# Optimization experiments

Measured on AMD Instinct MI355X. Metric: run time of the kernel, lower is better.

## Reference

```python
import jax, jax.numpy as jnp
import numpy as np

N = 100000   # nodes
E = 1600000  # edges
R = 20       # relations
B = 8        # bases
F_IN = 32
H = 32
F_OUT = 32


def _rel_layer(x, src, dst, etypes, V, a, w_loop, bias, activation=None):
    """DGL RelGraphConv with basis decomposition, sum aggregation, self-loop, bias.

    message m_e = x[src_e] @ W_{r_e}, W_r = sum_b a[r,b] V[b]; h_v = sum_{e->v} m_e
    Since messages are linear in x, aggregate x[src] per (dst, rel) segment first,
    then apply the relation weights once per node: same math, far less traffic.
    """
    W = jnp.einsum('rb,bio->rio', a, V)                       # [R, in, out]
    seg = dst.astype(jnp.int32) * R + etypes.astype(jnp.int32)  # [E]
    agg = jax.ops.segment_sum(x[src], seg, num_segments=N * R)  # [N*R, in]
    agg = agg.reshape(N, R, -1)
    h = jnp.einsum('nri,rio->no', agg, W) + x @ w_loop + bias   # [N, out]
    if activation is not None:
        h = activation(h)
    return h


def setup_inputs() -> dict:
    key = jax.random.key(0)
    ks = jax.random.split(key, 10)
    s = 1.0 / np.sqrt(F_IN)
    return {
        'x': jax.random.normal(ks[0], (N, F_IN), dtype=jnp.float32),
        'src': jax.random.randint(ks[1], (E,), 0, N, dtype=jnp.int32),
        'dst': jax.random.randint(ks[2], (E,), 0, N, dtype=jnp.int32),
        'etypes': jax.random.randint(ks[3], (E,), 0, R, dtype=jnp.int32),
        'V1': jax.random.normal(ks[4], (B, F_IN, H), dtype=jnp.float32) * s,
        'a1': jax.random.normal(ks[5], (R, B), dtype=jnp.float32) * s,
        'loop1': jax.random.normal(ks[6], (F_IN, H), dtype=jnp.float32) * s,
        'b1': jnp.zeros((H,), dtype=jnp.float32),
        'V2': jax.random.normal(ks[7], (B, H, F_OUT), dtype=jnp.float32) * s,
        'a2': jax.random.normal(ks[8], (R, B), dtype=jnp.float32) * s,
        'loop2': jax.random.normal(ks[9], (H, F_OUT), dtype=jnp.float32) * s,
        'b2': jnp.zeros((F_OUT,), dtype=jnp.float32),
    }


def reference(x, src, dst, etypes, V1, a1, loop1, b1, V2, a2, loop2, b2):
    h = _rel_layer(x, src, dst, etypes, V1, a1, loop1, b1, activation=jax.nn.relu)
    h = _rel_layer(h, src, dst, etypes, V2, a2, loop2, b2, activation=None)
    return h
```

## Files before the change

kernel.cpp:

```cpp
#include <hip/hip_runtime.h>
#include <hip/hip_bf16.h>

#define NN 100000
#define NE 1600000
#define NR 20
#define NB 8
#define FD 32


typedef short short8 __attribute__((ext_vector_type(8)));
typedef float f32x4  __attribute__((ext_vector_type(4)));

__device__ __forceinline__ unsigned short f2bf(float f) {
  union { float f; unsigned u; } c; c.f = f;
  unsigned r = c.u + 0x7FFF + ((c.u >> 16) & 1);
  return (unsigned short)(r >> 16);
}

__global__ void k_hist(const int* __restrict__ dst, int* __restrict__ hist) {
  int e = blockIdx.x * 256 + threadIdx.x;
  if (e < NE) atomicAdd(&hist[dst[e]], 1);
}

__global__ void k_scan1(int* __restrict__ data, int* __restrict__ aux, int n) {
  __shared__ int sd[256];
  int t = threadIdx.x, blk = blockIdx.x;
  int base = blk * 1024 + t * 4;
  int v[4];
#pragma unroll
  for (int j = 0; j < 4; ++j) v[j] = (base + j < n) ? data[base + j] : 0;
  int s = v[0] + v[1] + v[2] + v[3];
  sd[t] = s;
  __syncthreads();
  for (int off = 1; off < 256; off <<= 1) {
    int x = (t >= off) ? sd[t - off] : 0;
    __syncthreads();
    sd[t] += x;
    __syncthreads();
  }
  int run = sd[t] - s;
  if (t == 255) aux[blk] = sd[255];
#pragma unroll
  for (int j = 0; j < 4; ++j) {
    if (base + j < n) { data[base + j] = run; run += v[j]; }
  }
}

__global__ void k_scan2(int* __restrict__ aux, int n) {
  __shared__ int sd[256];
  int t = threadIdx.x;
  int loc[9];
  int s = 0;
#pragma unroll
  for (int j = 0; j < 9; ++j) {
    int idx = t * 9 + j;
    int v = (idx < n) ? aux[idx] : 0;
    loc[j] = s;
    s += v;
  }
  sd[t] = s;
  __syncthreads();
  for (int off = 1; off < 256; off <<= 1) {
    int x = (t >= off) ? sd[t - off] : 0;
    __syncthreads();
    sd[t] += x;
    __syncthreads();
  }
  int excl = sd[t] - s;
#pragma unroll
  for (int j = 0; j < 9; ++j) {
    int idx = t * 9 + j;
    if (idx < n) aux[idx] = excl + loc[j];
  }
}

__global__ void k_scan3(int* __restrict__ data, const int* __restrict__ aux, int n) {
  int i = blockIdx.x * 256 + threadIdx.x;
  if (i < n) data[i] += aux[i >> 10];
}

__global__ void k_scatter(const int* __restrict__ src, const int* __restrict__ dst,
                          const int* __restrict__ et, int* __restrict__ offs,
                          int* __restrict__ es) {
  int e = blockIdx.x * 256 + threadIdx.x;
  if (e >= NE) return;
  int pos = atomicAdd(&offs[dst[e]], 1);
  es[pos] = (src[e] << 5) | et[e];
}

__global__ void k_bfrag(const float* __restrict__ V1, const float* __restrict__ lp1,
                        const float* __restrict__ V2, const float* __restrict__ lp2,
                        unsigned short* __restrict__ Bf1, unsigned short* __restrict__ Bf2) {
  int t = blockIdx.x * 256 + threadIdx.x;
  if (t >= 2 * 9216) return;
  int layer = t / 9216;
  int idx = t - layer * 9216;
  int kstep = idx >> 10;
  int rem = idx & 1023;
  int otile = rem >> 9;
  int li = (rem >> 3) & 63;
  int j = idx & 7;
  int k = kstep * 32 + ((li >> 4) << 3) + j;
  int o = otile * 16 + (li & 15);
  const float* V = layer ? V2 : V1;
  const float* lp = layer ? lp2 : lp1;
  float val = (k < 256) ? V[k * 32 + o] : lp[(k - 256) * 32 + o];
  (layer ? Bf2 : Bf1)[idx] = f2bf(val);
}

__global__ void __launch_bounds__(256) k_edge(const float* __restrict__ xin,
                                              const int* __restrict__ offs,
                                              const int* __restrict__ es,
                                              const float* __restrict__ arel,
                                              unsigned short* __restrict__ zb,
                                              int n0, int n1) {
  int wid = (blockIdx.x * 256 + threadIdx.x) >> 6;
  int nw  = (gridDim.x * 256) >> 6;
  int l = threadIdx.x & 63;
  int i = l & 31, hh = l >> 5;
  const float4* aT = reinterpret_cast<const float4*>(arel);
  for (int v = n0 + wid; v < n1; v += nw) {
    int e0 = (v == 0) ? 0 : offs[v - 1];
    int e1 = offs[v];
    e0 = __builtin_amdgcn_readfirstlane(e0);
    e1 = __builtin_amdgcn_readfirstlane(e1);
    float z0 = 0.f, z1 = 0.f, z2 = 0.f, z3 = 0.f;
    int e = e0;
    for (; e + 8 <= e1; e += 8) {
      int r0 = es[e],     r1 = es[e + 1], r2 = es[e + 2], r3 = es[e + 3];
      int r4 = es[e + 4], r5 = es[e + 5], r6 = es[e + 6], r7 = es[e + 7];
      float x0 = xin[((r0 >> 5) << 5) | i];
      float x1 = xin[((r1 >> 5) << 5) | i];
      float x2 = xin[((r2 >> 5) << 5) | i];
      float x3 = xin[((r3 >> 5) << 5) | i];
      float x4 = xin[((r4 >> 5) << 5) | i];
      float x5 = xin[((r5 >> 5) << 5) | i];
      float x6 = xin[((r6 >> 5) << 5) | i];
      float x7 = xin[((r7 >> 5) << 5) | i];
      float4 a0 = aT[((r0 & 31) << 1) | hh];
      float4 a1 = aT[((r1 & 31) << 1) | hh];
      float4 a2 = aT[((r2 & 31) << 1) | hh];
      float4 a3 = aT[((r3 & 31) << 1) | hh];
      float4 a4 = aT[((r4 & 31) << 1) | hh];
      float4 a5 = aT[((r5 & 31) << 1) | hh];
      float4 a6 = aT[((r6 & 31) << 1) | hh];
      float4 a7 = aT[((r7 & 31) << 1) | hh];
      z0 += a0.x * x0; z1 += a0.y * x0; z2 += a0.z * x0; z3 += a0.w * x0;
      z0 += a1.x * x1; z1 += a1.y * x1; z2 += a1.z * x1; z3 += a1.w * x1;
      z0 += a2.x * x2; z1 += a2.y * x2; z2 += a2.z * x2; z3 += a2.w * x2;
      z0 += a3.x * x3; z1 += a3.y * x3; z2 += a3.z * x3; z3 += a3.w * x3;
      z0 += a4.x * x4; z1 += a4.y * x4; z2 += a4.z * x4; z3 += a4.w * x4;
      z0 += a5.x * x5; z1 += a5.y * x5; z2 += a5.z * x5; z3 += a5.w * x5;
      z0 += a6.x * x6; z1 += a6.y * x6; z2 += a6.z * x6; z3 += a6.w * x6;
      z0 += a7.x * x7; z1 += a7.y * x7; z2 += a7.z * x7; z3 += a7.w * x7;
    }
    for (; e + 4 <= e1; e += 4) {
      int r0 = es[e], r1 = es[e + 1], r2 = es[e + 2], r3 = es[e + 3];
      float x0 = xin[((r0 >> 5) << 5) | i];
      float x1 = xin[((r1 >> 5) << 5) | i];
      float x2 = xin[((r2 >> 5) << 5) | i];
      float x3 = xin[((r3 >> 5) << 5) | i];
      float4 a0 = aT[((r0 & 31) << 1) | hh];
      float4 a1 = aT[((r1 & 31) << 1) | hh];
      float4 a2 = aT[((r2 & 31) << 1) | hh];
      float4 a3 = aT[((r3 & 31) << 1) | hh];
      z0 += a0.x * x0; z1 += a0.y * x0; z2 += a0.z * x0; z3 += a0.w * x0;
      z0 += a1.x * x1; z1 += a1.y * x1; z2 += a1.z * x1; z3 += a1.w * x1;
      z0 += a2.x * x2; z1 += a2.y * x2; z2 += a2.z * x2; z3 += a2.w * x2;
      z0 += a3.x * x3; z1 += a3.y * x3; z2 += a3.z * x3; z3 += a3.w * x3;
    }
    for (; e < e1; ++e) {
      int rec = es[e];
      int s = rec >> 5, r = rec & 31;
      float xv = xin[(s << 5) | i];
      float4 av = aT[(r << 1) | hh];
      z0 += av.x * xv; z1 += av.y * xv; z2 += av.z * xv; z3 += av.w * xv;
    }
    unsigned short* zp = zb + ((size_t)(v - n0) << 8) + (hh << 7) + i;
    zp[0]  = f2bf(z0);
    zp[32] = f2bf(z1);
    zp[64] = f2bf(z2);
    zp[96] = f2bf(z3);
  }
}

__global__ void __launch_bounds__(256) k_finish(const unsigned short* __restrict__ zb,
                                                const float* __restrict__ xin,
                                                const unsigned short* __restrict__ Bfrag,
                                                const float* __restrict__ bias,
                                                float* __restrict__ hout,
                                                int n0, int n1, int do_relu) {
  int lane = threadIdx.x & 63;
  int wid = (blockIdx.x * 256 + threadIdx.x) >> 6;
  int nwv = (gridDim.x * 256) >> 6;
  const short8* Bp = reinterpret_cast<const short8*>(Bfrag);
  short8 bf[9][2];
#pragma unroll
  for (int ks = 0; ks < 9; ++ks)
#pragma unroll
    for (int ot = 0; ot < 2; ++ot)
      bf[ks][ot] = Bp[((ks * 2 + ot) << 6) + lane];
  float bsv0 = bias[lane & 15];
  float bsv1 = bias[16 + (lane & 15)];
  int cnt = n1 - n0;
  int tiles = (cnt + 15) >> 4;
  int row = lane & 15;
  int kg = lane >> 4;
  for (int t = wid; t < tiles; t += nwv) {
    int nb = t << 4;
    int r = nb + row;
    int rc = (r < cnt) ? r : (cnt - 1);
    const short8* zrow = reinterpret_cast<const short8*>(zb + ((size_t)rc << 8));
    f32x4 acc0 = {0.f, 0.f, 0.f, 0.f};
    f32x4 acc1 = {0.f, 0.f, 0.f, 0.f};
#pragma unroll
    for (int ks = 0; ks < 8; ++ks) {
      short8 af = zrow[(ks << 2) + kg];
      acc0 = __builtin_amdgcn_mfma_f32_16x16x32_bf16(af, bf[ks][0], acc0, 0, 0, 0);
      acc1 = __builtin_amdgcn_mfma_f32_16x16x32_bf16(af, bf[ks][1], acc1, 0, 0, 0);
    }
    {
      const float4* xr = reinterpret_cast<const float4*>(xin + ((size_t)(n0 + rc) << 5) + (kg << 3));
      float4 xa = xr[0], xb2 = xr[1];
      short8 xs;
      xs[0] = (short)f2bf(xa.x);  xs[1] = (short)f2bf(xa.y);
      xs[2] = (short)f2bf(xa.z);  xs[3] = (short)f2bf(xa.w);
      xs[4] = (short)f2bf(xb2.x); xs[5] = (short)f2bf(xb2.y);
      xs[6] = (short)f2bf(xb2.z); xs[7] = (short)f2bf(xb2.w);
      acc0 = __builtin_amdgcn_mfma_f32_16x16x32_bf16(xs, bf[8][0], acc0, 0, 0, 0);
      acc1 = __builtin_amdgcn_mfma_f32_16x16x32_bf16(xs, bf[8][1], acc1, 0, 0, 0);
    }
#pragma unroll
    for (int q = 0; q < 4; ++q) {
      int orow = (kg << 2) + q;
      int n = nb + orow;
      if (n < cnt) {
        float v0 = acc0[q] + bsv0;
        float v1 = acc1[q] + bsv1;
        if (do_relu) { v0 = fmaxf(v0, 0.f); v1 = fmaxf(v1, 0.f); }
        float* hp = hout + ((size_t)(n0 + n) << 5);
        hp[row] = v0;
        hp[16 + row] = v1;
      }
    }
  }
}

extern "C" void kernel_launch(void* const* d_in, const int* in_sizes, int n_in,
                              void* d_out, int out_size, void* d_ws, size_t ws_size,
                              hipStream_t stream) {
  const float* x   = (const float*)d_in[0];
  const int* src   = (const int*)d_in[1];
  const int* dst   = (const int*)d_in[2];
  const int* et    = (const int*)d_in[3];
  const float* V1  = (const float*)d_in[4];
  const float* a1  = (const float*)d_in[5];
  const float* lp1 = (const float*)d_in[6];
  const float* b1  = (const float*)d_in[7];
  const float* V2  = (const float*)d_in[8];
  const float* a2  = (const float*)d_in[9];
  const float* lp2 = (const float*)d_in[10];
  const float* b2  = (const float*)d_in[11];
  float* out = (float*)d_out;

  char* w = (char*)d_ws;
  int* offs = (int*)(w + 0);
  int* aux  = (int*)(w + 400128);
  int* es   = (int*)(w + 400640);
  float* h1 = (float*)(w + 6800640);
  unsigned short* Bf1 = (unsigned short*)(w + 19600640);
  unsigned short* Bf2 = (unsigned short*)(w + 19619072);
  const size_t ZB_OFF = 19637504;
  if (ws_size < ZB_OFF + (size_t)4096 * 512) return;
  unsigned short* zb = (unsigned short*)(w + ZB_OFF);
  int cap = (int)((ws_size - ZB_OFF) / 512);
  if (cap > NN) cap = NN;
  int nch = (NN + cap - 1) / cap;
  int cs  = (((NN + nch - 1) / nch) + 15) & ~15;

  hipMemsetAsync(offs, 0, (size_t)NN * 4, stream);

  k_hist<<<(NE + 255) / 256, 256, 0, stream>>>(dst, offs);

  int nScanBlk = (NN + 1023) / 1024;
  k_scan1<<<nScanBlk, 256, 0, stream>>>(offs, aux, NN);
  k_scan2<<<1, 256, 0, stream>>>(aux, nScanBlk);
  k_scan3<<<(NN + 255) / 256, 256, 0, stream>>>(offs, aux, NN);

  k_scatter<<<(NE + 255) / 256, 256, 0, stream>>>(src, dst, et, offs, es);

  k_bfrag<<<(2 * 9216 + 255) / 256, 256, 0, stream>>>(V1, lp1, V2, lp2, Bf1, Bf2);

  for (int c = 0; c < nch; ++c) {
    int n0 = c * cs, n1 = n0 + cs;
    if (n1 > NN) n1 = NN;
    if (n0 >= n1) break;
    int tiles = ((n1 - n0) + 15) >> 4;
    int fblk = (tiles + 3) / 4; if (fblk > 512) fblk = 512;
    k_edge<<<2048, 256, 0, stream>>>(x, offs, es, a1, zb, n0, n1);
    k_finish<<<fblk, 256, 0, stream>>>(zb, x, Bf1, b1, h1, n0, n1, 1);
  }
  for (int c = 0; c < nch; ++c) {
    int n0 = c * cs, n1 = n0 + cs;
    if (n1 > NN) n1 = NN;
    if (n0 >= n1) break;
    int tiles = ((n1 - n0) + 15) >> 4;
    int fblk = (tiles + 3) / 4; if (fblk > 512) fblk = 512;
    k_edge<<<2048, 256, 0, stream>>>(h1, offs, es, a2, zb, n0, n1);
    k_finish<<<fblk, 256, 0, stream>>>(zb, h1, Bf2, b2, out, n0, n1, 0);
  }
}
```

Measured before the change: 473.1 us.

## Replace global-atomic CSR scatter with LDS bucket sort and gather bf16 features

The edge-to-CSR construction now bins edges by destination block in shared memory and then places them per bucket with shared-memory atomics, replacing per-edge global atomics and random writes. Input features and the hidden layer are stored in bf16, so the per-edge gathers in the edge kernel move half the bytes and the finish kernel loads bf16 directly. This adds extra kernels, a binning buffer, and bf16 rounding of the intermediate activations.

After: 423.4 us. 1.12x faster.

```diff
diff --git a/kernel.cpp b/kernel.cpp
--- a/kernel.cpp
+++ b/kernel.cpp
@@ -7,6 +7,9 @@
 #define NB 8
 #define FD 32
 
+#define EPB 8192
+#define NBB ((NE + EPB - 1) / EPB)
+#define NBKT ((NN + 255) / 256)
 
 typedef short short8 __attribute__((ext_vector_type(8)));
 typedef float f32x4  __attribute__((ext_vector_type(4)));
@@ -15,6 +18,9 @@
   union { float f; unsigned u; } c; c.f = f;
   unsigned r = c.u + 0x7FFF + ((c.u >> 16) & 1);
   return (unsigned short)(r >> 16);
+}
+__device__ __forceinline__ float bf2f(unsigned short u) {
+  union { unsigned u; float f; } c; c.u = ((unsigned)u) << 16; return c.f;
 }
 
 __global__ void k_hist(const int* __restrict__ dst, int* __restrict__ hist) {
@@ -79,13 +85,87 @@
   if (i < n) data[i] += aux[i >> 10];
 }
 
-__global__ void k_scatter(const int* __restrict__ src, const int* __restrict__ dst,
-                          const int* __restrict__ et, int* __restrict__ offs,
-                          int* __restrict__ es) {
-  int e = blockIdx.x * 256 + threadIdx.x;
-  if (e >= NE) return;
-  int pos = atomicAdd(&offs[dst[e]], 1);
-  es[pos] = (src[e] << 5) | et[e];
+__global__ void k_endcap(int* __restrict__ ioffs) {
+  if (threadIdx.x == 0 && blockIdx.x == 0) ioffs[NN] = NE;
+}
+
+__global__ void __launch_bounds__(256) k_bin(const int* __restrict__ src,
+                                             const int* __restrict__ dst,
+                                             const int* __restrict__ et,
+                                             int* __restrict__ binbuf,
+                                             int* __restrict__ bcnt,
+                                             int* __restrict__ segoff) {
+  __shared__ int sA[512], sB[512];
+  int g = blockIdx.x, t = threadIdx.x;
+  int e0 = g * EPB;
+  int e1 = e0 + EPB; if (e1 > NE) e1 = NE;
+  sA[t] = 0; sA[t + 256] = 0;
+  __syncthreads();
+  for (int e = e0 + t; e < e1; e += 256) atomicAdd(&sA[dst[e] >> 8], 1);
+  __syncthreads();
+  for (int b = t; b < NBKT; b += 256) bcnt[g * NBKT + b] = sA[b];
+  int* pa = sA; int* pb = sB;
+  for (int off = 1; off < 512; off <<= 1) {
+    __syncthreads();
+    for (int idx = t; idx < 512; idx += 256) {
+      int v = pa[idx];
+      if (idx >= off) v += pa[idx - off];
+      pb[idx] = v;
+    }
+    int* tmp = pa; pa = pb; pb = tmp;
+  }
+  __syncthreads();
+  for (int b = t; b < NBKT; b += 256) {
+    int ex = b ? pa[b - 1] : 0;
+    segoff[g * NBKT + b] = e0 + ex;
+    pb[b] = ex;
+  }
+  __syncthreads();
+  for (int e = e0 + t; e < e1; e += 256) {
+    int d = dst[e];
+    int pos = atomicAdd(&pb[d >> 8], 1);
+    binbuf[e0 + pos] = (src[e] << 13) | ((d & 255) << 5) | et[e];
+  }
+}
+
+__global__ void __launch_bounds__(256) k_bsort(const int* __restrict__ binbuf,
+                                               const int* __restrict__ bcnt,
+                                               const int* __restrict__ segoff,
+                                               const int* __restrict__ ioffs,
+                                               int* __restrict__ es) {
+  __shared__ int cur[256];
+  __shared__ int scnt[NBB], ssof[NBB];
+  int b = blockIdx.x, t = threadIdx.x;
+  int node = b * 256 + t;
+  cur[t] = (node < NN) ? ioffs[node] : 0;
+  for (int g = t; g < NBB; g += 256) {
+    scnt[g] = bcnt[g * NBKT + b];
+    ssof[g] = segoff[g * NBKT + b];
+  }
+  __syncthreads();
+  int w = t >> 6, l = t & 63;
+  for (int g = w; g < NBB; g += 4) {
+    int c = scnt[g], so = ssof[g];
+    for (int base = l; base < c; base += 64) {
+      int v = binbuf[so + base];
+      int j = (v >> 5) & 255;
+      int pos = atomicAdd(&cur[j], 1);
+      es[pos] = ((v >> 13) << 5) | (v & 31);
+    }
+  }
+}
+
+__global__ void k_xcast(const float* __restrict__ x, unsigned short* __restrict__ xb) {
+  int t = blockIdx.x * 256 + threadIdx.x;
+  if (t >= (NN * FD) / 8) return;
+  const float4* xp = reinterpret_cast<const float4*>(x) + t * 2;
+  float4 a = xp[0], b = xp[1];
+  short8 v;
+  v[0] = (short)f2bf(a.x); v[1] = (short)f2bf(a.y);
+  v[2] = (short)f2bf(a.z); v[3] = (short)f2bf(a.w);
+  v[4] = (short)f2bf(b.x); v[5] = (short)f2bf(b.y);
+  v[6] = (short)f2bf(b.z); v[7] = (short)f2bf(b.w);
+  reinterpret_cast<short8*>(xb)[t] = v;
 }
 
 __global__ void k_bfrag(const float* __restrict__ V1, const float* __restrict__ lp1,
@@ -108,8 +188,8 @@
   (layer ? Bf2 : Bf1)[idx] = f2bf(val);
 }
 
-__global__ void __launch_bounds__(256) k_edge(const float* __restrict__ xin,
-                                              const int* __restrict__ offs,
+__global__ void __launch_bounds__(256) k_edge(const unsigned short* __restrict__ xin,
+                                              const int* __restrict__ ioffs,
                                               const int* __restrict__ es,
                                               const float* __restrict__ arel,
                                               unsigned short* __restrict__ zb,
@@ -120,23 +200,21 @@
   int i = l & 31, hh = l >> 5;
   const float4* aT = reinterpret_cast<const float4*>(arel);
   for (int v = n0 + wid; v < n1; v += nw) {
-    int e0 = (v == 0) ? 0 : offs[v - 1];
-    int e1 = offs[v];
-    e0 = __builtin_amdgcn_readfirstlane(e0);
-    e1 = __builtin_amdgcn_readfirstlane(e1);
+    int e0 = __builtin_amdgcn_readfirstlane(ioffs[v]);
+    int e1 = __builtin_amdgcn_readfirstlane(ioffs[v + 1]);
     float z0 = 0.f, z1 = 0.f, z2 = 0.f, z3 = 0.f;
     int e = e0;
     for (; e + 8 <= e1; e += 8) {
       int r0 = es[e],     r1 = es[e + 1], r2 = es[e + 2], r3 = es[e + 3];
       int r4 = es[e + 4], r5 = es[e + 5], r6 = es[e + 6], r7 = es[e + 7];
-      float x0 = xin[((r0 >> 5) << 5) | i];
-      float x1 = xin[((r1 >> 5) << 5) | i];
-      float x2 = xin[((r2 >> 5) << 5) | i];
-      float x3 = xin[((r3 >> 5) << 5) | i];
-      float x4 = xin[((r4 >> 5) << 5) | i];
-      float x5 = xin[((r5 >> 5) << 5) | i];
-      float x6 = xin[((r6 >> 5) << 5) | i];
-      float x7 = xin[((r7 >> 5) << 5) | i];
+      float x0 = bf2f(xin[((r0 >> 5) << 5) | i]);
+      float x1 = bf2f(xin[((r1 >> 5) << 5) | i]);
+      float x2 = bf2f(xin[((r2 >> 5) << 5) | i]);
+      float x3 = bf2f(xin[((r3 >> 5) << 5) | i]);
+      float x4 = bf2f(xin[((r4 >> 5) << 5) | i]);
+      float x5 = bf2f(xin[((r5 >> 5) << 5) | i]);
+      float x6 = bf2f(xin[((r6 >> 5) << 5) | i]);
+      float x7 = bf2f(xin[((r7 >> 5) << 5) | i]);
       float4 a0 = aT[((r0 & 31) << 1) | hh];
       float4 a1 = aT[((r1 & 31) << 1) | hh];
       float4 a2 = aT[((r2 & 31) << 1) | hh];
@@ -156,10 +234,10 @@
     }
     for (; e + 4 <= e1; e += 4) {
       int r0 = es[e], r1 = es[e + 1], r2 = es[e + 2], r3 = es[e + 3];
-      float x0 = xin[((r0 >> 5) << 5) | i];
-      float x1 = xin[((r1 >> 5) << 5) | i];
-      float x2 = xin[((r2 >> 5) << 5) | i];
-      float x3 = xin[((r3 >> 5) << 5) | i];
+      float x0 = bf2f(xin[((r0 >> 5) << 5) | i]);
+      float x1 = bf2f(xin[((r1 >> 5) << 5) | i]);
+      float x2 = bf2f(xin[((r2 >> 5) << 5) | i]);
+      float x3 = bf2f(xin[((r3 >> 5) << 5) | i]);
       float4 a0 = aT[((r0 & 31) << 1) | hh];
       float4 a1 = aT[((r1 & 31) << 1) | hh];
       float4 a2 = aT[((r2 & 31) << 1) | hh];
@@ -171,9 +249,8 @@
     }
     for (; e < e1; ++e) {
       int rec = es[e];
-      int s = rec >> 5, r = rec & 31;
-      float xv = xin[(s << 5) | i];
-      float4 av = aT[(r << 1) | hh];
+      float xv = bf2f(xin[((rec >> 5) << 5) | i]);
+      float4 av = aT[((rec & 31) << 1) | hh];
       z0 += av.x * xv; z1 += av.y * xv; z2 += av.z * xv; z3 += av.w * xv;
     }
     unsigned short* zp = zb + ((size_t)(v - n0) << 8) + (hh << 7) + i;
@@ -185,10 +262,11 @@
 }
 
 __global__ void __launch_bounds__(256) k_finish(const unsigned short* __restrict__ zb,
-                                                const float* __restrict__ xin,
+                                                const unsigned short* __restrict__ xin,
                                                 const unsigned short* __restrict__ Bfrag,
                                                 const float* __restrict__ bias,
-                                                float* __restrict__ hout,
+                                                float* __restrict__ out_f32,
+                                                unsigned short* __restrict__ out_bf16,
                                                 int n0, int n1, int do_relu) {
   int lane = threadIdx.x & 63;
   int wid = (blockIdx.x * 256 + threadIdx.x) >> 6;
@@ -220,13 +298,7 @@
       acc1 = __builtin_amdgcn_mfma_f32_16x16x32_bf16(af, bf[ks][1], acc1, 0, 0, 0);
     }
     {
-      const float4* xr = reinterpret_cast<const float4*>(xin + ((size_t)(n0 + rc) << 5) + (kg << 3));
-      float4 xa = xr[0], xb2 = xr[1];
-      short8 xs;
-      xs[0] = (short)f2bf(xa.x);  xs[1] = (short)f2bf(xa.y);
-      xs[2] = (short)f2bf(xa.z);  xs[3] = (short)f2bf(xa.w);
-      xs[4] = (short)f2bf(xb2.x); xs[5] = (short)f2bf(xb2.y);
-      xs[6] = (short)f2bf(xb2.z); xs[7] = (short)f2bf(xb2.w);
+      short8 xs = *reinterpret_cast<const short8*>(xin + ((size_t)(n0 + rc) << 5) + (kg << 3));
       acc0 = __builtin_amdgcn_mfma_f32_16x16x32_bf16(xs, bf[8][0], acc0, 0, 0, 0);
       acc1 = __builtin_amdgcn_mfma_f32_16x16x32_bf16(xs, bf[8][1], acc1, 0, 0, 0);
     }
@@ -238,9 +310,9 @@
         float v0 = acc0[q] + bsv0;
         float v1 = acc1[q] + bsv1;
         if (do_relu) { v0 = fmaxf(v0, 0.f); v1 = fmaxf(v1, 0.f); }
-        float* hp = hout + ((size_t)(n0 + n) << 5);
-        hp[row] = v0;
-        hp[16 + row] = v1;
+        size_t base = ((size_t)(n0 + n) << 5);
+        if (out_f32) { out_f32[base + row] = v0; out_f32[base + 16 + row] = v1; }
+        if (out_bf16) { out_bf16[base + row] = f2bf(v0); out_bf16[base + 16 + row] = f2bf(v1); }
       }
     }
   }
@@ -264,13 +336,17 @@
   float* out = (float*)d_out;
 
   char* w = (char*)d_ws;
-  int* offs = (int*)(w + 0);
-  int* aux  = (int*)(w + 400128);
-  int* es   = (int*)(w + 400640);
-  float* h1 = (float*)(w + 6800640);
-  unsigned short* Bf1 = (unsigned short*)(w + 19600640);
-  unsigned short* Bf2 = (unsigned short*)(w + 19619072);
-  const size_t ZB_OFF = 19637504;
+  int* ioffs = (int*)(w + 0);
+  int* aux   = (int*)(w + 400128);
+  int* es    = (int*)(w + 400640);
+  int* binbuf= (int*)(w + 6800640);
+  int* bcnt  = (int*)(w + 13223168);
+  int* segoff= (int*)(w + 13529728);
+  unsigned short* xb  = (unsigned short*)(w + 13836288);
+  unsigned short* h1b = (unsigned short*)(w + 20236288);
+  unsigned short* Bf1 = (unsigned short*)(w + 26636288);
+  unsigned short* Bf2 = (unsigned short*)(w + 26654720);
+  const size_t ZB_OFF = 26673152;
   if (ws_size < ZB_OFF + (size_t)4096 * 512) return;
   unsigned short* zb = (unsigned short*)(w + ZB_OFF);
   int cap = (int)((ws_size - ZB_OFF) / 512);
@@ -278,17 +354,20 @@
   int nch = (NN + cap - 1) / cap;
   int cs  = (((NN + nch - 1) / nch) + 15) & ~15;
 
-  hipMemsetAsync(offs, 0, (size_t)NN * 4, stream);
-
-  k_hist<<<(NE + 255) / 256, 256, 0, stream>>>(dst, offs);
+  hipMemsetAsync(ioffs, 0, (size_t)NN * 4, stream);
+
+  k_hist<<<(NE + 255) / 256, 256, 0, stream>>>(dst, ioffs);
 
   int nScanBlk = (NN + 1023) / 1024;
-  k_scan1<<<nScanBlk, 256, 0, stream>>>(offs, aux, NN);
+  k_scan1<<<nScanBlk, 256, 0, stream>>>(ioffs, aux, NN);
   k_scan2<<<1, 256, 0, stream>>>(aux, nScanBlk);
-  k_scan3<<<(NN + 255) / 256, 256, 0, stream>>>(offs, aux, NN);
-
-  k_scatter<<<(NE + 255) / 256, 256, 0, stream>>>(src, dst, et, offs, es);
-
+  k_scan3<<<(NN + 255) / 256, 256, 0, stream>>>(ioffs, aux, NN);
+  k_endcap<<<1, 64, 0, stream>>>(ioffs);
+
+  k_bin<<<NBB, 256, 0, stream>>>(src, dst, et, binbuf, bcnt, segoff);
+  k_bsort<<<NBKT, 256, 0, stream>>>(binbuf, bcnt, segoff, ioffs, es);
+
+  k_xcast<<<((NN * FD / 8) + 255) / 256, 256, 0, stream>>>(x, xb);
   k_bfrag<<<(2 * 9216 + 255) / 256, 256, 0, stream>>>(V1, lp1, V2, lp2, Bf1, Bf2);
 
   for (int c = 0; c < nch; ++c) {
@@ -297,8 +376,8 @@
     if (n0 >= n1) break;
     int tiles = ((n1 - n0) + 15) >> 4;
     int fblk = (tiles + 3) / 4; if (fblk > 512) fblk = 512;
-    k_edge<<<2048, 256, 0, stream>>>(x, offs, es, a1, zb, n0, n1);
-    k_finish<<<fblk, 256, 0, stream>>>(zb, x, Bf1, b1, h1, n0, n1, 1);
+    k_edge<<<2048, 256, 0, stream>>>(xb, ioffs, es, a1, zb, n0, n1);
+    k_finish<<<fblk, 256, 0, stream>>>(zb, xb, Bf1, b1, nullptr, h1b, n0, n1, 1);
   }
   for (int c = 0; c < nch; ++c) {
     int n0 = c * cs, n1 = n0 + cs;
@@ -306,7 +385,7 @@
     if (n0 >= n1) break;
     int tiles = ((n1 - n0) + 15) >> 4;
     int fblk = (tiles + 3) / 4; if (fblk > 512) fblk = 512;
-    k_edge<<<2048, 256, 0, stream>>>(h1, offs, es, a2, zb, n0, n1);
-    k_finish<<<fblk, 256, 0, stream>>>(zb, h1, Bf2, b2, out, n0, n1, 0);
-  }
-}
+    k_edge<<<2048, 256, 0, stream>>>(h1b, ioffs, es, a2, zb, n0, n1);
+    k_finish<<<fblk, 256, 0, stream>>>(zb, h1b, Bf2, b2, out, nullptr, n0, n1, 0);
+  }
+}
```
